# Kernel optimization log

Hardware: AMD Instinct MI355X
Metric: run time of the kernel (lower is better)

Reference implementation:

```python
import jax, jax.numpy as jnp
import numpy as np

T, H, I, E, K = 1024, 1024, 1024, 16, 8
INIT_STD = 0.02


def setup_inputs() -> dict:
    key = jax.random.key(0)
    k0, k1, k2, k3, k4 = jax.random.split(key, 5)
    hidden_states = jax.random.normal(k0, (T, H), dtype=jnp.float32)
    top_k_index = jax.random.randint(k1, (T, K), 0, E, dtype=jnp.int64)
    top_k_weights = jax.random.uniform(k2, (T, K), dtype=jnp.float32)
    gate_up_proj = jax.random.normal(k3, (E, 2 * I, H), dtype=jnp.float32) * INIT_STD
    down_proj = jax.random.normal(k4, (E, H, I), dtype=jnp.float32) * INIT_STD
    return {
        "hidden_states": hidden_states,
        "top_k_index": top_k_index,
        "top_k_weights": top_k_weights,
        "gate_up_proj": gate_up_proj,
        "down_proj": down_proj,
    }


def reference(hidden_states, top_k_index, top_k_weights, gate_up_proj, down_proj):
    # hidden_states: [T, H]; gate_up_proj: [E, 2I, H]; down_proj: [E, H, I]
    num_tokens = hidden_states.shape[0]
    num_experts = gate_up_proj.shape[0]

    # Per-token combine weights: scatter top_k_weights into a dense [T, E] map.
    # Tokens not routed to expert e get weight 0, so the dense all-expert
    # compute below is mathematically identical to the masked gather/scatter loop.
    token_ids = jnp.arange(num_tokens)[:, None]  # [T, 1]
    combine = jnp.zeros((num_tokens, num_experts), dtype=hidden_states.dtype)
    combine = combine.at[token_ids, top_k_index].add(top_k_weights)  # [T, E]

    # Gated MLP for every (token, expert) pair.
    gate_up = jnp.einsum("th,eoh->teo", hidden_states, gate_up_proj)  # [T, E, 2I]
    gate, up = jnp.split(gate_up, 2, axis=-1)
    act = jax.nn.silu(gate) * up  # [T, E, I]
    down = jnp.einsum("tei,ehi->teh", act, down_proj)  # [T, E, H]

    # Weighted combine over experts (zero weight -> no contribution).
    return jnp.einsum("teh,te->th", down, combine)  # [T, H]
```

## Files before the change

### kernel.cpp

```cpp
#include <hip/hip_runtime.h>
#include <cstdint>
#include <cstddef>

#define TT 1024
#define HH 1024
#define IW 1024
#define EE 16
#define KK 8
#define NSLOT (TT*KK)
#define NTMAX 80

typedef unsigned short u16;
typedef unsigned int   u32;
typedef __attribute__((ext_vector_type(4))) float f32x4;
typedef __attribute__((ext_vector_type(8))) short s16x8;
typedef __attribute__((ext_vector_type(8))) u16   u16x8;

__device__ __forceinline__ u16 f2bf(float f) {
  union { float f; u32 u; } v; v.f = f;
  u32 u = v.u + 0x7fffu + ((v.u >> 16) & 1u);
  return (u16)(u >> 16);
}

__device__ __forceinline__ void gload16(const void* g, void* l) {
  __builtin_amdgcn_global_load_lds(
      (const __attribute__((address_space(1))) u32*)g,
      (__attribute__((address_space(3))) u32*)l, 16, 0, 0);
}

#define MFMA16(a, b, c) __builtin_amdgcn_mfma_f32_16x16x32_bf16((a), (b), (c), 0, 0, 0)


__global__ void k_cvt(const float* __restrict__ src, u16* __restrict__ dst) {
  int g = blockIdx.x * 256 + threadIdx.x;
  const f32x4* s = (const f32x4*)(src + (size_t)g * 8);
  f32x4 f0 = s[0], f1 = s[1];
  u16x8 p;
#pragma unroll
  for (int i = 0; i < 4; ++i) { p[i] = f2bf(f0[i]); p[i + 4] = f2bf(f1[i]); }
  *(u16x8*)(dst + (size_t)g * 8) = p;
}

__global__ void k_count(const int* __restrict__ idx, int* __restrict__ counts) {
  for (int s = blockIdx.x * 256 + threadIdx.x; s < NSLOT; s += gridDim.x * 256)
    atomicAdd(&counts[idx[s]], 1);
}

__global__ void k_scan(const int* __restrict__ counts, int* __restrict__ offsets,
                       int* __restrict__ cursor, int* __restrict__ tile_e,
                       int* __restrict__ tile_mt) {
  if (threadIdx.x == 0) {
    int r = 0, t = 0;
    for (int e = 0; e < EE; ++e) {
      offsets[e] = r; cursor[e] = r;
      int c = counts[e];
      for (int mt = 0; mt * 128 < c; ++mt) { tile_e[t] = e; tile_mt[t] = mt; ++t; }
      r += c;
    }
    offsets[EE] = r;
    for (; t < NTMAX; ++t) tile_e[t] = -1;
  }
}

__global__ void k_scatter(const int* __restrict__ idx, const float* __restrict__ tkw,
                          int* __restrict__ cursor, int* __restrict__ slot_token,
                          float* __restrict__ slot_w, int* __restrict__ inv) {
  for (int s = blockIdx.x * 256 + threadIdx.x; s < NSLOT; s += gridDim.x * 256) {
    int e = idx[s];
    int pos = atomicAdd(&cursor[e], 1);
    slot_token[pos] = s >> 3;
    slot_w[pos] = tkw[s];
    inv[s] = pos;
  }
}


__global__ __launch_bounds__(256, 2) void k_gemm1(
    const u16* __restrict__ xb,
    const u16* __restrict__ gupb,
    const int* __restrict__ offsets,
    const int* __restrict__ slot_token,
    const float* __restrict__ slot_w,
    const int* __restrict__ tile_e,
    const int* __restrict__ tile_mt,
    u16* __restrict__ act)
{
  __shared__ __align__(16) u16 As[128 * 32];
  __shared__ __align__(16) u16 Bgs[64 * 32];
  __shared__ __align__(16) u16 Bus[64 * 32];

  const int e = tile_e[blockIdx.y];
  if (e < 0) return;
  const int mt = tile_mt[blockIdx.y], nt = blockIdx.x;
  const int off = offsets[e];
  const int ne  = offsets[e + 1] - off;

  const int tid = threadIdx.x;
  const int lane = tid & 63, wid = tid >> 6;
  const int wm = wid >> 1, wn = wid & 1;

  const int l4 = lane >> 2;
  const int lq = lane & 3;
  const int chunk = lq ^ ((l4 >> 1) & 3);

  const u16* asrc[2];
#pragma unroll
  for (int q = 0; q < 2; ++q) {
    int grow = mt * 128 + q * 64 + wid * 16 + l4;
    if (grow >= ne) grow = ne - 1;
    asrc[q] = xb + (size_t)slot_token[off + grow] * HH + chunk * 8;
  }
  const int bch = nt * 64 + wid * 16 + l4;
  const u16* bgsrc = gupb + ((size_t)e * 2 * IW + bch) * HH + chunk * 8;
  const u16* busrc = bgsrc + (size_t)IW * HH;
  u16* const adst0 = As + (0 * 64 + wid * 16) * 32;
  u16* const adst1 = As + (1 * 64 + wid * 16) * 32;
  u16* const bgdst = Bgs + (wid * 16) * 32;
  u16* const budst = Bus + (wid * 16) * 32;

  f32x4 accg[4][2], accu[4][2];
  const f32x4 zz = {0.f, 0.f, 0.f, 0.f};
#pragma unroll
  for (int m = 0; m < 4; ++m)
#pragma unroll
    for (int n = 0; n < 2; ++n) { accg[m][n] = zz; accu[m][n] = zz; }

  const int r16 = lane & 15, kg = lane >> 4;
  const int rq = ((kg ^ ((r16 >> 1) & 3)) << 3);

  for (int kk = 0; kk < HH / 32; ++kk) {
    const int k0 = kk * 32;
    gload16(asrc[0] + k0, adst0);
    gload16(asrc[1] + k0, adst1);
    gload16(bgsrc + k0, bgdst);
    gload16(busrc + k0, budst);
    __syncthreads();

    s16x8 a[4], bg[2], bu[2];
#pragma unroll
    for (int m = 0; m < 4; ++m)
      a[m] = *(const s16x8*)(As + (wm * 64 + m * 16 + r16) * 32 + rq);
#pragma unroll
    for (int n = 0; n < 2; ++n) {
      bg[n] = *(const s16x8*)(Bgs + (wn * 32 + n * 16 + r16) * 32 + rq);
      bu[n] = *(const s16x8*)(Bus + (wn * 32 + n * 16 + r16) * 32 + rq);
    }
#pragma unroll
    for (int m = 0; m < 4; ++m)
#pragma unroll
      for (int n = 0; n < 2; ++n) {
        accg[m][n] = MFMA16(a[m], bg[n], accg[m][n]);
        accu[m][n] = MFMA16(a[m], bu[n], accu[m][n]);
      }
    __syncthreads();
  }

#pragma unroll
  for (int m = 0; m < 4; ++m) {
    const int baserow = mt * 128 + wm * 64 + m * 16 + kg * 4;
#pragma unroll
    for (int n = 0; n < 2; ++n) {
      const int c = nt * 64 + wn * 32 + n * 16 + r16;
#pragma unroll
      for (int j = 0; j < 4; ++j) {
        const int row = baserow + j;
        if (row < ne) {
          float g = accg[m][n][j], u = accu[m][n][j];
          float sv = g / (1.f + __expf(-g));
          act[(size_t)(off + row) * IW + c] = f2bf(sv * u * slot_w[off + row]);
        }
      }
    }
  }
}


__global__ __launch_bounds__(256, 2) void k_gemm2(
    const u16* __restrict__ act,
    const u16* __restrict__ dpb,
    const int* __restrict__ offsets,
    const int* __restrict__ tile_e,
    const int* __restrict__ tile_mt,
    float* __restrict__ wdown)
{
  __shared__ __align__(16) u16 As[128 * 32];
  __shared__ __align__(16) u16 Bs[128 * 32];

  const int e = tile_e[blockIdx.y];
  if (e < 0) return;
  const int mt = tile_mt[blockIdx.y], nt = blockIdx.x;
  const int off = offsets[e];
  const int ne  = offsets[e + 1] - off;

  const int tid = threadIdx.x;
  const int lane = tid & 63, wid = tid >> 6;
  const int wm = wid >> 1, wn = wid & 1;

  const int l4 = lane >> 2, lq = lane & 3;
  const int chunk = lq ^ ((l4 >> 1) & 3);

  const u16* asrc[2];
#pragma unroll
  for (int q = 0; q < 2; ++q) {
    int grow = mt * 128 + q * 64 + wid * 16 + l4;
    if (grow >= ne) grow = ne - 1;
    asrc[q] = act + (size_t)(off + grow) * IW + chunk * 8;
  }
  const u16* bsrc[2];
#pragma unroll
  for (int q = 0; q < 2; ++q)
    bsrc[q] = dpb + ((size_t)e * HH + nt * 128 + q * 64 + wid * 16 + l4) * IW + chunk * 8;

  u16* const adst0 = As + (0 * 64 + wid * 16) * 32;
  u16* const adst1 = As + (1 * 64 + wid * 16) * 32;
  u16* const bdst0 = Bs + (0 * 64 + wid * 16) * 32;
  u16* const bdst1 = Bs + (1 * 64 + wid * 16) * 32;

  f32x4 acc[4][4];
  const f32x4 zz = {0.f, 0.f, 0.f, 0.f};
#pragma unroll
  for (int m = 0; m < 4; ++m)
#pragma unroll
    for (int n = 0; n < 4; ++n) acc[m][n] = zz;

  const int r16 = lane & 15, kg = lane >> 4;
  const int rq = ((kg ^ ((r16 >> 1) & 3)) << 3);

  for (int kk = 0; kk < IW / 32; ++kk) {
    const int k0 = kk * 32;
    gload16(asrc[0] + k0, adst0);
    gload16(asrc[1] + k0, adst1);
    gload16(bsrc[0] + k0, bdst0);
    gload16(bsrc[1] + k0, bdst1);
    __syncthreads();

    s16x8 a[4], b[4];
#pragma unroll
    for (int m = 0; m < 4; ++m)
      a[m] = *(const s16x8*)(As + (wm * 64 + m * 16 + r16) * 32 + rq);
#pragma unroll
    for (int n = 0; n < 4; ++n)
      b[n] = *(const s16x8*)(Bs + (wn * 64 + n * 16 + r16) * 32 + rq);
#pragma unroll
    for (int m = 0; m < 4; ++m)
#pragma unroll
      for (int n = 0; n < 4; ++n)
        acc[m][n] = MFMA16(a[m], b[n], acc[m][n]);
    __syncthreads();
  }

#pragma unroll
  for (int m = 0; m < 4; ++m) {
    const int baserow = mt * 128 + wm * 64 + m * 16 + kg * 4;
#pragma unroll
    for (int n = 0; n < 4; ++n) {
      const int h = nt * 128 + wn * 64 + n * 16 + r16;
#pragma unroll
      for (int j = 0; j < 4; ++j) {
        const int row = baserow + j;
        if (row < ne)
          wdown[(size_t)(off + row) * HH + h] = acc[m][n][j];
      }
    }
  }
}


__global__ void k_combine(const float* __restrict__ wdown, const int* __restrict__ inv,
                          float* __restrict__ out) {
  int g = blockIdx.x * 256 + threadIdx.x;
  int t = g >> 8;
  int hv = (g & 255) * 4;
  f32x4 a = {0.f, 0.f, 0.f, 0.f};
#pragma unroll
  for (int k = 0; k < KK; ++k) {
    int pos = inv[t * KK + k];
    f32x4 v = *(const f32x4*)(wdown + (size_t)pos * HH + hv);
    a += v;
  }
  *(f32x4*)(out + (size_t)t * HH + hv) = a;
}


extern "C" void kernel_launch(void* const* d_in, const int* in_sizes, int n_in,
                              void* d_out, int out_size, void* d_ws, size_t ws_size,
                              hipStream_t stream) {
  const float* hs  = (const float*)d_in[0];
  const int*   idx = (const int*)d_in[1];
  const float* tkw = (const float*)d_in[2];
  const float* gup = (const float*)d_in[3];
  const float* dpw = (const float*)d_in[4];
  float* out = (float*)d_out;

  char* ws = (char*)d_ws;
  size_t o = 0;
  u16* xb   = (u16*)(ws + o);       o += (size_t)TT * HH * 2;
  u16* gupb = (u16*)(ws + o);       o += (size_t)EE * 2 * IW * HH * 2;
  u16* dpb  = (u16*)(ws + o);       o += (size_t)EE * HH * IW * 2;
  int* counts  = (int*)(ws + o);    o += 64;
  int* cursor  = (int*)(ws + o);    o += 64;
  int* offsets = (int*)(ws + o);    o += 128;
  int* tile_e  = (int*)(ws + o);    o += NTMAX * 4;
  int* tile_mt = (int*)(ws + o);    o += NTMAX * 4;
  int* slot_token = (int*)(ws + o); o += (size_t)NSLOT * 4;
  int* inv     = (int*)(ws + o);    o += (size_t)NSLOT * 4;
  float* slot_w = (float*)(ws + o); o += (size_t)NSLOT * 4;
  o = (o + 255) & ~(size_t)255;
  u16* act = (u16*)(ws + o);        o += (size_t)NSLOT * IW * 2;
  float* wdown = (float*)(ws + o);  o += (size_t)NSLOT * HH * 4;

  hipMemsetAsync(counts, 0, 64, stream);
  k_cvt<<<TT * HH / (256 * 8), 256, 0, stream>>>(hs, xb);
  k_cvt<<<(int)((size_t)EE * 2 * IW * HH / (256 * 8)), 256, 0, stream>>>(gup, gupb);
  k_cvt<<<(int)((size_t)EE * HH * IW / (256 * 8)), 256, 0, stream>>>(dpw, dpb);
  k_count<<<16, 256, 0, stream>>>(idx, counts);
  k_scan<<<1, 64, 0, stream>>>(counts, offsets, cursor, tile_e, tile_mt);
  k_scatter<<<16, 256, 0, stream>>>(idx, tkw, cursor, slot_token, slot_w, inv);
  k_gemm1<<<dim3(IW / 64, NTMAX), 256, 0, stream>>>(xb, gupb, offsets, slot_token,
                                                    slot_w, tile_e, tile_mt, act);
  k_gemm2<<<dim3(HH / 128, NTMAX), 256, 0, stream>>>(act, dpb, offsets, tile_e, tile_mt, wdown);
  k_combine<<<TT * HH / 4 / 256, 256, 0, stream>>>(wdown, inv, out);
}
```

Baseline: 410.5 us.

## Double-buffer GEMM tiles, fuse routing and conversion kernels, store down output in bf16

```diff
diff --git a/kernel.cpp b/kernel.cpp
--- a/kernel.cpp
+++ b/kernel.cpp
@@ -21,6 +21,10 @@
   u32 u = v.u + 0x7fffu + ((v.u >> 16) & 1u);
   return (u16)(u >> 16);
 }
+__device__ __forceinline__ float bf2f(u16 b) {
+  union { u32 u; float f; } v; v.u = (u32)b << 16;
+  return v.f;
+}
 
 __device__ __forceinline__ void gload16(const void* g, void* l) {
   __builtin_amdgcn_global_load_lds(
@@ -31,49 +35,58 @@
 #define MFMA16(a, b, c) __builtin_amdgcn_mfma_f32_16x16x32_bf16((a), (b), (c), 0, 0, 0)
 
 
-__global__ void k_cvt(const float* __restrict__ src, u16* __restrict__ dst) {
-  int g = blockIdx.x * 256 + threadIdx.x;
-  const f32x4* s = (const f32x4*)(src + (size_t)g * 8);
+__global__ void k_cvt_all(const float* __restrict__ hs, const float* __restrict__ gup,
+                          const float* __restrict__ dp, u16* __restrict__ xb,
+                          u16* __restrict__ gupb, u16* __restrict__ dpb) {
+  int b = blockIdx.x;
+  const float* src; u16* dst; size_t rel;
+  if (b < 512)        { src = hs;  dst = xb;   rel = (size_t)b; }
+  else if (b < 16896) { src = gup; dst = gupb; rel = (size_t)(b - 512); }
+  else                { src = dp;  dst = dpb;  rel = (size_t)(b - 16896); }
+  size_t g = rel * 2048 + (size_t)threadIdx.x * 8;
+  const f32x4* s = (const f32x4*)(src + g);
   f32x4 f0 = s[0], f1 = s[1];
   u16x8 p;
 #pragma unroll
   for (int i = 0; i < 4; ++i) { p[i] = f2bf(f0[i]); p[i + 4] = f2bf(f1[i]); }
-  *(u16x8*)(dst + (size_t)g * 8) = p;
-}
-
-__global__ void k_count(const int* __restrict__ idx, int* __restrict__ counts) {
-  for (int s = blockIdx.x * 256 + threadIdx.x; s < NSLOT; s += gridDim.x * 256)
-    atomicAdd(&counts[idx[s]], 1);
-}
-
-__global__ void k_scan(const int* __restrict__ counts, int* __restrict__ offsets,
-                       int* __restrict__ cursor, int* __restrict__ tile_e,
-                       int* __restrict__ tile_mt) {
-  if (threadIdx.x == 0) {
+  *(u16x8*)(dst + g) = p;
+}
+
+
+__global__ void k_route(const int* __restrict__ idx, const float* __restrict__ tkw,
+                        int* __restrict__ offsets, int* __restrict__ slot_token,
+                        float* __restrict__ slot_w, int* __restrict__ inv,
+                        int* __restrict__ tile_e, int* __restrict__ tile_mt) {
+  __shared__ int cnt[EE], cur[EE];
+  const int tid = threadIdx.x;
+  if (tid < EE) cnt[tid] = 0;
+  __syncthreads();
+  for (int s = tid; s < NSLOT; s += 256) atomicAdd(&cnt[idx[s]], 1);
+  __syncthreads();
+  if (tid == 0) {
     int r = 0, t = 0;
     for (int e = 0; e < EE; ++e) {
-      offsets[e] = r; cursor[e] = r;
-      int c = counts[e];
+      offsets[e] = r; cur[e] = r;
+      int c = cnt[e];
       for (int mt = 0; mt * 128 < c; ++mt) { tile_e[t] = e; tile_mt[t] = mt; ++t; }
       r += c;
     }
     offsets[EE] = r;
     for (; t < NTMAX; ++t) tile_e[t] = -1;
   }
-}
-
-__global__ void k_scatter(const int* __restrict__ idx, const float* __restrict__ tkw,
-                          int* __restrict__ cursor, int* __restrict__ slot_token,
-                          float* __restrict__ slot_w, int* __restrict__ inv) {
-  for (int s = blockIdx.x * 256 + threadIdx.x; s < NSLOT; s += gridDim.x * 256) {
+  __syncthreads();
+  for (int s = tid; s < NSLOT; s += 256) {
     int e = idx[s];
-    int pos = atomicAdd(&cursor[e], 1);
+    int pos = atomicAdd(&cur[e], 1);
     slot_token[pos] = s >> 3;
     slot_w[pos] = tkw[s];
     inv[s] = pos;
   }
 }
 
+
+#define G1_ASZ (128*32)
+#define G1_BSZ (64*32)
 
 __global__ __launch_bounds__(256, 2) void k_gemm1(
     const u16* __restrict__ xb,
@@ -85,9 +98,9 @@
     const int* __restrict__ tile_mt,
     u16* __restrict__ act)
 {
-  __shared__ __align__(16) u16 As[128 * 32];
-  __shared__ __align__(16) u16 Bgs[64 * 32];
-  __shared__ __align__(16) u16 Bus[64 * 32];
+  __shared__ __align__(16) u16 As[2 * G1_ASZ];
+  __shared__ __align__(16) u16 Bgs[2 * G1_BSZ];
+  __shared__ __align__(16) u16 Bus[2 * G1_BSZ];
 
   const int e = tile_e[blockIdx.y];
   if (e < 0) return;
@@ -113,10 +126,9 @@
   const int bch = nt * 64 + wid * 16 + l4;
   const u16* bgsrc = gupb + ((size_t)e * 2 * IW + bch) * HH + chunk * 8;
   const u16* busrc = bgsrc + (size_t)IW * HH;
-  u16* const adst0 = As + (0 * 64 + wid * 16) * 32;
-  u16* const adst1 = As + (1 * 64 + wid * 16) * 32;
-  u16* const bgdst = Bgs + (wid * 16) * 32;
-  u16* const budst = Bus + (wid * 16) * 32;
+  const int ad0 = (0 * 64 + wid * 16) * 32;
+  const int ad1 = (1 * 64 + wid * 16) * 32;
+  const int bd  = (wid * 16) * 32;
 
   f32x4 accg[4][2], accu[4][2];
   const f32x4 zz = {0.f, 0.f, 0.f, 0.f};
@@ -128,22 +140,33 @@
   const int r16 = lane & 15, kg = lane >> 4;
   const int rq = ((kg ^ ((r16 >> 1) & 3)) << 3);
 
+  gload16(asrc[0], As + ad0);
+  gload16(asrc[1], As + ad1);
+  gload16(bgsrc,   Bgs + bd);
+  gload16(busrc,   Bus + bd);
+  __syncthreads();
+
   for (int kk = 0; kk < HH / 32; ++kk) {
-    const int k0 = kk * 32;
-    gload16(asrc[0] + k0, adst0);
-    gload16(asrc[1] + k0, adst1);
-    gload16(bgsrc + k0, bgdst);
-    gload16(busrc + k0, budst);
-    __syncthreads();
+    const int cur = kk & 1;
+    if (kk + 1 < HH / 32) {
+      const int nb = cur ^ 1, k0 = (kk + 1) * 32;
+      gload16(asrc[0] + k0, As + nb * G1_ASZ + ad0);
+      gload16(asrc[1] + k0, As + nb * G1_ASZ + ad1);
+      gload16(bgsrc   + k0, Bgs + nb * G1_BSZ + bd);
+      gload16(busrc   + k0, Bus + nb * G1_BSZ + bd);
+    }
+    const u16* Ab  = As  + cur * G1_ASZ;
+    const u16* Bgb = Bgs + cur * G1_BSZ;
+    const u16* Bub = Bus + cur * G1_BSZ;
 
     s16x8 a[4], bg[2], bu[2];
 #pragma unroll
     for (int m = 0; m < 4; ++m)
-      a[m] = *(const s16x8*)(As + (wm * 64 + m * 16 + r16) * 32 + rq);
+      a[m] = *(const s16x8*)(Ab + (wm * 64 + m * 16 + r16) * 32 + rq);
 #pragma unroll
     for (int n = 0; n < 2; ++n) {
-      bg[n] = *(const s16x8*)(Bgs + (wn * 32 + n * 16 + r16) * 32 + rq);
-      bu[n] = *(const s16x8*)(Bus + (wn * 32 + n * 16 + r16) * 32 + rq);
+      bg[n] = *(const s16x8*)(Bgb + (wn * 32 + n * 16 + r16) * 32 + rq);
+      bu[n] = *(const s16x8*)(Bub + (wn * 32 + n * 16 + r16) * 32 + rq);
     }
 #pragma unroll
     for (int m = 0; m < 4; ++m)
@@ -175,16 +198,18 @@
 }
 
 
+#define G2_SZ (128*32)
+
 __global__ __launch_bounds__(256, 2) void k_gemm2(
     const u16* __restrict__ act,
     const u16* __restrict__ dpb,
     const int* __restrict__ offsets,
     const int* __restrict__ tile_e,
     const int* __restrict__ tile_mt,
-    float* __restrict__ wdown)
+    u16* __restrict__ wdown)
 {
-  __shared__ __align__(16) u16 As[128 * 32];
-  __shared__ __align__(16) u16 Bs[128 * 32];
+  __shared__ __align__(16) u16 As[2 * G2_SZ];
+  __shared__ __align__(16) u16 Bs[2 * G2_SZ];
 
   const int e = tile_e[blockIdx.y];
   if (e < 0) return;
@@ -211,10 +236,8 @@
   for (int q = 0; q < 2; ++q)
     bsrc[q] = dpb + ((size_t)e * HH + nt * 128 + q * 64 + wid * 16 + l4) * IW + chunk * 8;
 
-  u16* const adst0 = As + (0 * 64 + wid * 16) * 32;
-  u16* const adst1 = As + (1 * 64 + wid * 16) * 32;
-  u16* const bdst0 = Bs + (0 * 64 + wid * 16) * 32;
-  u16* const bdst1 = Bs + (1 * 64 + wid * 16) * 32;
+  const int d0 = (0 * 64 + wid * 16) * 32;
+  const int d1 = (1 * 64 + wid * 16) * 32;
 
   f32x4 acc[4][4];
   const f32x4 zz = {0.f, 0.f, 0.f, 0.f};
@@ -226,21 +249,31 @@
   const int r16 = lane & 15, kg = lane >> 4;
   const int rq = ((kg ^ ((r16 >> 1) & 3)) << 3);
 
+  gload16(asrc[0], As + d0);
+  gload16(asrc[1], As + d1);
+  gload16(bsrc[0], Bs + d0);
+  gload16(bsrc[1], Bs + d1);
+  __syncthreads();
+
   for (int kk = 0; kk < IW / 32; ++kk) {
-    const int k0 = kk * 32;
-    gload16(asrc[0] + k0, adst0);
-    gload16(asrc[1] + k0, adst1);
-    gload16(bsrc[0] + k0, bdst0);
-    gload16(bsrc[1] + k0, bdst1);
-    __syncthreads();
+    const int cur = kk & 1;
+    if (kk + 1 < IW / 32) {
+      const int nb = cur ^ 1, k0 = (kk + 1) * 32;
+      gload16(asrc[0] + k0, As + nb * G2_SZ + d0);
+      gload16(asrc[1] + k0, As + nb * G2_SZ + d1);
+      gload16(bsrc[0] + k0, Bs + nb * G2_SZ + d0);
+      gload16(bsrc[1] + k0, Bs + nb * G2_SZ + d1);
+    }
+    const u16* Ab = As + cur * G2_SZ;
+    const u16* Bb = Bs + cur * G2_SZ;
 
     s16x8 a[4], b[4];
 #pragma unroll
     for (int m = 0; m < 4; ++m)
-      a[m] = *(const s16x8*)(As + (wm * 64 + m * 16 + r16) * 32 + rq);
+      a[m] = *(const s16x8*)(Ab + (wm * 64 + m * 16 + r16) * 32 + rq);
 #pragma unroll
     for (int n = 0; n < 4; ++n)
-      b[n] = *(const s16x8*)(Bs + (wn * 64 + n * 16 + r16) * 32 + rq);
+      b[n] = *(const s16x8*)(Bb + (wn * 64 + n * 16 + r16) * 32 + rq);
 #pragma unroll
     for (int m = 0; m < 4; ++m)
 #pragma unroll
@@ -259,26 +292,31 @@
       for (int j = 0; j < 4; ++j) {
         const int row = baserow + j;
         if (row < ne)
-          wdown[(size_t)(off + row) * HH + h] = acc[m][n][j];
+          wdown[(size_t)(off + row) * HH + h] = f2bf(acc[m][n][j]);
       }
     }
   }
 }
 
 
-__global__ void k_combine(const float* __restrict__ wdown, const int* __restrict__ inv,
+__global__ void k_combine(const u16* __restrict__ wdown, const int* __restrict__ inv,
                           float* __restrict__ out) {
   int g = blockIdx.x * 256 + threadIdx.x;
-  int t = g >> 8;
-  int hv = (g & 255) * 4;
-  f32x4 a = {0.f, 0.f, 0.f, 0.f};
+  int t = g >> 7;
+  int hv = (g & 127) * 8;
+  const int* ip = inv + t * KK;
+  float acc[8] = {0.f, 0.f, 0.f, 0.f, 0.f, 0.f, 0.f, 0.f};
 #pragma unroll
   for (int k = 0; k < KK; ++k) {
-    int pos = inv[t * KK + k];
-    f32x4 v = *(const f32x4*)(wdown + (size_t)pos * HH + hv);
-    a += v;
-  }
-  *(f32x4*)(out + (size_t)t * HH + hv) = a;
+    int pos = ip[k];
+    u16x8 v = *(const u16x8*)(wdown + (size_t)pos * HH + hv);
+#pragma unroll
+    for (int j = 0; j < 8; ++j) acc[j] += bf2f(v[j]);
+  }
+  f32x4 o0 = {acc[0], acc[1], acc[2], acc[3]};
+  f32x4 o1 = {acc[4], acc[5], acc[6], acc[7]};
+  *(f32x4*)(out + (size_t)t * HH + hv)     = o0;
+  *(f32x4*)(out + (size_t)t * HH + hv + 4) = o1;
 }
 
 
@@ -297,8 +335,6 @@
   u16* xb   = (u16*)(ws + o);       o += (size_t)TT * HH * 2;
   u16* gupb = (u16*)(ws + o);       o += (size_t)EE * 2 * IW * HH * 2;
   u16* dpb  = (u16*)(ws + o);       o += (size_t)EE * HH * IW * 2;
-  int* counts  = (int*)(ws + o);    o += 64;
-  int* cursor  = (int*)(ws + o);    o += 64;
   int* offsets = (int*)(ws + o);    o += 128;
   int* tile_e  = (int*)(ws + o);    o += NTMAX * 4;
   int* tile_mt = (int*)(ws + o);    o += NTMAX * 4;
@@ -307,17 +343,14 @@
   float* slot_w = (float*)(ws + o); o += (size_t)NSLOT * 4;
   o = (o + 255) & ~(size_t)255;
   u16* act = (u16*)(ws + o);        o += (size_t)NSLOT * IW * 2;
-  float* wdown = (float*)(ws + o);  o += (size_t)NSLOT * HH * 4;
-
-  hipMemsetAsync(counts, 0, 64, stream);
-  k_cvt<<<TT * HH / (256 * 8), 256, 0, stream>>>(hs, xb);
-  k_cvt<<<(int)((size_t)EE * 2 * IW * HH / (256 * 8)), 256, 0, stream>>>(gup, gupb);
-  k_cvt<<<(int)((size_t)EE * HH * IW / (256 * 8)), 256, 0, stream>>>(dpw, dpb);
-  k_count<<<16, 256, 0, stream>>>(idx, counts);
-  k_scan<<<1, 64, 0, stream>>>(counts, offsets, cursor, tile_e, tile_mt);
-  k_scatter<<<16, 256, 0, stream>>>(idx, tkw, cursor, slot_token, slot_w, inv);
+  u16* wdown = (u16*)(ws + o);      o += (size_t)NSLOT * HH * 2;
+
+  k_route<<<1, 256, 0, stream>>>(idx, tkw, offsets, slot_token, slot_w, inv,
+                                 tile_e, tile_mt);
+  k_cvt_all<<<25088, 256, 0, stream>>>(hs, gup, dpw, xb, gupb, dpb);
   k_gemm1<<<dim3(IW / 64, NTMAX), 256, 0, stream>>>(xb, gupb, offsets, slot_token,
                                                     slot_w, tile_e, tile_mt, act);
-  k_gemm2<<<dim3(HH / 128, NTMAX), 256, 0, stream>>>(act, dpb, offsets, tile_e, tile_mt, wdown);
-  k_combine<<<TT * HH / 4 / 256, 256, 0, stream>>>(wdown, inv, out);
-}
+  k_gemm2<<<dim3(HH / 128, NTMAX), 256, 0, stream>>>(act, dpb, offsets, tile_e,
+                                                     tile_mt, wdown);
+  k_combine<<<TT * HH / 8 / 256, 256, 0, stream>>>(wdown, inv, out);
+}
```

New measurement: 387.3 us. -5.7%, faster.
